# Performance work log

Measured on AMD Instinct MI355X. Metric: run time of the kernel, lower is better.

Reference implementation:

```python
import jax, jax.numpy as jnp
import numpy as np

N_NUC = 100_000
N_NN = 1_600_000
EMB = 128
MSG = 32
OUT = 128
LN_EPS = 1e-6  # flax LayerNorm default


def setup_inputs() -> dict:
    key = jax.random.key(0)
    ks = jax.random.split(key, 12)
    inp = {
        "s_embed": jax.random.normal(ks[0], (N_NUC, EMB), jnp.float32),
        "r_embed": jax.random.normal(ks[1], (N_NUC, EMB), jnp.float32),
        "e_embed": jax.random.normal(ks[2], (N_NN, MSG), jnp.float32),
        "norm": jax.random.uniform(ks[3], (N_NUC,), jnp.float32),
        "senders": jax.random.randint(ks[4], (N_NN,), 0, N_NUC, jnp.int32),
        "receivers": jax.random.randint(ks[5], (N_NN,), 0, N_NUC, jnp.int32),
        # learned parameters
        "W_s": jax.random.normal(ks[6], (EMB, MSG), jnp.float32) / np.sqrt(EMB),
        "b_s": jnp.zeros((MSG,), jnp.float32),
        "W_r": jax.random.normal(ks[7], (EMB, MSG), jnp.float32) / np.sqrt(EMB),
        "b_r": jnp.zeros((MSG,), jnp.float32),
        "ln_scale": jnp.ones((MSG,), jnp.float32),
        "ln_bias": jnp.zeros((MSG,), jnp.float32),
        "W_e": jax.random.normal(ks[8], (MSG, MSG), jnp.float32) / np.sqrt(MSG),
        "W_out": jax.random.normal(ks[9], (MSG, OUT), jnp.float32) / np.sqrt(MSG),
    }
    return inp


def _layernorm(x, scale, bias):
    mu = jnp.mean(x, axis=-1, keepdims=True)
    var = jnp.mean(jnp.square(x - mu), axis=-1, keepdims=True)
    return (x - mu) * jax.lax.rsqrt(var + LN_EPS) * scale + bias


def reference(s_embed, r_embed, e_embed, norm, senders, receivers,
              W_s, b_s, W_r, b_r, ln_scale, ln_bias, W_e, W_out):
    # Dense projections on nodes, then gather per edge: [n_nn, msg]
    inp = (s_embed @ W_s + b_s)[senders] + (r_embed @ W_r + b_r)[receivers]
    inp = _layernorm(inp, ln_scale, ln_bias)
    inp = jax.nn.silu(inp)
    inp = inp * (e_embed @ W_e)  # elementwise edge gating
    # scatter-add to receivers: [n_nuc, msg]
    msg = jax.ops.segment_sum(inp, receivers, num_segments=s_embed.shape[0])
    msg = msg * norm[:, None]
    return jax.nn.silu(msg @ W_out)
```

## Files before the change

### kernel.cpp

```cpp
#include <hip/hip_runtime.h>
#include <hip/hip_bf16.h>
#include <math.h>

#define N_NUC_C 100000
#define N_NN_C  1600000
#define EMB_C   128
#define MSG_C   32
#define OUT_C   128
#define NB1     98
#define NPART   8
#define R_PER_P (N_NUC_C / NPART)
#define SBLK    784
#define STHREADS (SBLK * 256)
#define LDS_USTR 17

__device__ __forceinline__ float silu_f(float y) {
    return y / (1.0f + __expf(-y));
}

__device__ __forceinline__ unsigned pack_bf16x2(float a, float b) {
    unsigned ua = __float_as_uint(a); ua += 0x7FFFu + ((ua >> 16) & 1u);
    unsigned ub = __float_as_uint(b); ub += 0x7FFFu + ((ub >> 16) & 1u);
    return (ua >> 16) | (ub & 0xFFFF0000u);
}

__global__ __launch_bounds__(256) void proj_kernel(
    const float* __restrict__ s_embed, const float* __restrict__ r_embed,
    const float* __restrict__ W_s, const float* __restrict__ b_s,
    const float* __restrict__ W_r, const float* __restrict__ b_r,
    float* __restrict__ proj )
{
    const int n   = blockIdx.x * blockDim.x + threadIdx.x;
    const int sub = blockIdx.y;
    const int pr  = sub >> 1;
    const int c0  = (sub & 1) * 16;
    if (n >= N_NUC_C) return;

    const float* __restrict__ src = pr ? r_embed : s_embed;
    const float* __restrict__ W   = pr ? W_r : W_s;
    const float* __restrict__ b   = pr ? b_r : b_s;
    float* __restrict__ dst = proj + (size_t)pr * N_NUC_C * MSG_C;

    float acc[16];
    #pragma unroll
    for (int i = 0; i < 16; ++i) acc[i] = b[c0 + i];

    const float* row = src + (size_t)n * EMB_C;
    #pragma unroll 4
    for (int k = 0; k < EMB_C; k += 4) {
        const float4 rv = *reinterpret_cast<const float4*>(row + k);
        #pragma unroll
        for (int i = 0; i < 16; ++i) {
            acc[i] = fmaf(rv.x, W[(k + 0) * MSG_C + c0 + i], acc[i]);
            acc[i] = fmaf(rv.y, W[(k + 1) * MSG_C + c0 + i], acc[i]);
            acc[i] = fmaf(rv.z, W[(k + 2) * MSG_C + c0 + i], acc[i]);
            acc[i] = fmaf(rv.w, W[(k + 3) * MSG_C + c0 + i], acc[i]);
        }
    }

    float4* d = reinterpret_cast<float4*>(dst + (size_t)n * MSG_C + c0);
    d[0] = make_float4(acc[0],  acc[1],  acc[2],  acc[3]);
    d[1] = make_float4(acc[4],  acc[5],  acc[6],  acc[7]);
    d[2] = make_float4(acc[8],  acc[9],  acc[10], acc[11]);
    d[3] = make_float4(acc[12], acc[13], acc[14], acc[15]);
}

__global__ __launch_bounds__(256) void rank_kernel(
    const int* __restrict__ receivers, int* __restrict__ cnt,
    int* __restrict__ rank)
{
    const int e = blockIdx.x * blockDim.x + threadIdx.x;
    if (e >= N_NN_C) return;
    rank[e] = atomicAdd(&cnt[receivers[e]], 1);
}

__global__ __launch_bounds__(256) void scan1_kernel(
    const int* __restrict__ cnt, int* __restrict__ excl, int* __restrict__ blockTot)
{
    __shared__ int waveTot[4];
    const int t = threadIdx.x, b = blockIdx.x;
    const int lane = t & 63, wid = t >> 6;
    const int base = b * 1024 + t * 4;

    int d0 = (base + 0 < N_NUC_C) ? cnt[base + 0] : 0;
    int d1 = (base + 1 < N_NUC_C) ? cnt[base + 1] : 0;
    int d2 = (base + 2 < N_NUC_C) ? cnt[base + 2] : 0;
    int d3 = (base + 3 < N_NUC_C) ? cnt[base + 3] : 0;
    const int s = d0 + d1 + d2 + d3;

    int incl = s;
    #pragma unroll
    for (int off = 1; off < 64; off <<= 1) {
        int v = __shfl_up(incl, off);
        if (lane >= off) incl += v;
    }
    const int wexcl = incl - s;
    if (lane == 63) waveTot[wid] = incl;
    __syncthreads();
    int wbase = 0;
    for (int w = 0; w < wid; ++w) wbase += waveTot[w];
    const int e0 = wbase + wexcl;

    if (base + 0 < N_NUC_C) excl[base + 0] = e0;
    if (base + 1 < N_NUC_C) excl[base + 1] = e0 + d0;
    if (base + 2 < N_NUC_C) excl[base + 2] = e0 + d0 + d1;
    if (base + 3 < N_NUC_C) excl[base + 3] = e0 + d0 + d1 + d2;
    if (t == 255) blockTot[b] = wbase + incl;
}

__global__ __launch_bounds__(128) void scan2_kernel(
    const int* __restrict__ blockTot, int* __restrict__ blockOff)
{
    __shared__ int sh[128];
    const int t = threadIdx.x;
    const int v = (t < NB1) ? blockTot[t] : 0;
    sh[t] = v;
    __syncthreads();
    #pragma unroll
    for (int off = 1; off < 128; off <<= 1) {
        int x = 0;
        if (t >= off) x = sh[t - off];
        __syncthreads();
        sh[t] += x;
        __syncthreads();
    }
    if (t < NB1) blockOff[t] = sh[t] - v;
}

__global__ __launch_bounds__(256) void scan3_kernel(
    const int* __restrict__ excl, const int* __restrict__ blockOff,
    int* __restrict__ offsets)
{
    const int n = blockIdx.x * blockDim.x + threadIdx.x;
    if (n < N_NUC_C) offsets[n] = excl[n] + blockOff[n >> 10];
    if (n == 0) offsets[N_NUC_C] = N_NN_C;
}

__global__ __launch_bounds__(256) void scatter_pack8_kernel(
    const int* __restrict__ senders, const int* __restrict__ receivers,
    const int* __restrict__ rank, const int* __restrict__ offsets,
    int4* __restrict__ edge_pack)
{
    const int p    = blockIdx.x & 7;
    const int blk  = blockIdx.x >> 3;
    const int base = blk * 256 + threadIdx.x;
    const int rlo  = p * R_PER_P;
    const int rhi  = rlo + R_PER_P;

    #pragma unroll
    for (int k = 0; k < 8; ++k) {
        const int e = base + k * STHREADS;
        if (e < N_NN_C) {
            const int r = receivers[e];
            if (r >= rlo && r < rhi) {
                const int dst = offsets[r] + rank[e];
                edge_pack[dst] = make_int4(e, senders[e], r, 0);
            }
        }
    }
}

__global__ __launch_bounds__(256) void fused_csr_kernel(
    const float* __restrict__ proj,
    const float* __restrict__ e_embed,
    const int4*  __restrict__ edge_pack,
    const int*   __restrict__ offsets,
    const float* __restrict__ ln_scale,
    const float* __restrict__ ln_bias,
    const float* __restrict__ W_e,
    float*       __restrict__ msg)
{
    __shared__ unsigned lds_u[256 * LDS_USTR];
    __shared__ int      lds_r[256];

    const int t  = threadIdx.x;
    const int B0 = blockIdx.x * 256;

    const int4 pk = edge_pack[B0 + t];
    const int e = pk.x, s = pk.y, r = pk.z;
    lds_r[t] = r;

    const float4* ee = reinterpret_cast<const float4*>(e_embed + (size_t)e * MSG_C);
    const float4* ps = reinterpret_cast<const float4*>(proj + (size_t)s * MSG_C);
    const float4* pq = reinterpret_cast<const float4*>(proj + (size_t)(N_NUC_C + r) * MSG_C);

    float ev[MSG_C], x[MSG_C];
    #pragma unroll
    for (int q = 0; q < 8; ++q) {
        const float4 v = ee[q];
        ev[4*q+0] = v.x; ev[4*q+1] = v.y; ev[4*q+2] = v.z; ev[4*q+3] = v.w;
    }
    #pragma unroll
    for (int q = 0; q < 8; ++q) {
        const float4 a = ps[q];
        const float4 b = pq[q];
        x[4*q+0] = a.x + b.x; x[4*q+1] = a.y + b.y;
        x[4*q+2] = a.z + b.z; x[4*q+3] = a.w + b.w;
    }

    float g[MSG_C];
    #pragma unroll
    for (int c = 0; c < MSG_C; ++c) g[c] = 0.0f;
    #pragma unroll
    for (int k = 0; k < MSG_C; ++k) {
        const float ek = ev[k];
        #pragma unroll
        for (int c = 0; c < MSG_C; ++c)
            g[c] = fmaf(ek, W_e[k * MSG_C + c], g[c]);
    }

    float mu = 0.0f;
    #pragma unroll
    for (int c = 0; c < MSG_C; ++c) mu += x[c];
    mu *= (1.0f / MSG_C);
    float var = 0.0f;
    #pragma unroll
    for (int c = 0; c < MSG_C; ++c) { const float d = x[c] - mu; var = fmaf(d, d, var); }
    var *= (1.0f / MSG_C);
    const float rs = rsqrtf(var + 1e-6f);

    unsigned* orow = &lds_u[t * LDS_USTR];
    #pragma unroll
    for (int i = 0; i < 16; ++i) {
        const int c0_ = 2*i, c1_ = 2*i + 1;
        const float y0 = (x[c0_] - mu) * rs * ln_scale[c0_] + ln_bias[c0_];
        const float y1 = (x[c1_] - mu) * rs * ln_scale[c1_] + ln_bias[c1_];
        orow[i] = pack_bf16x2(silu_f(y0) * g[c0_], silu_f(y1) * g[c1_]);
    }

    __syncthreads();

    const int r0 = lds_r[0];
    const int r1 = lds_r[255];
    const int total = (r1 - r0 + 1) << 5;

    for (int p = t; p < total; p += 256) {
        const int n  = r0 + (p >> 5);
        const int ch = p & 31;
        int b  = offsets[n];
        int en = offsets[n + 1];
        const bool interior = (b >= B0) && (en <= B0 + 256);
        if (b < B0) b = B0;
        if (en > B0 + 256) en = B0 + 256;

        const int dw  = ch >> 1;
        const bool hi = (ch & 1);
        float sum = 0.0f;
        for (int q = b - B0; q < en - B0; ++q) {
            const unsigned u = lds_u[q * LDS_USTR + dw];
            sum += __uint_as_float(hi ? (u & 0xFFFF0000u) : (u << 16));
        }

        float* dst = msg + (size_t)n * MSG_C + ch;
        if (interior)       *dst = sum;
        else if (en > b)    atomicAdd(dst, sum);
    }
}

__global__ __launch_bounds__(256) void edge_kernel(
    const float* __restrict__ proj, const float* __restrict__ e_embed,
    const int* __restrict__ senders, const int* __restrict__ receivers,
    const float* __restrict__ ln_scale, const float* __restrict__ ln_bias,
    const float* __restrict__ W_e, float* __restrict__ msg)
{
    const int e = blockIdx.x * blockDim.x + threadIdx.x;
    if (e >= N_NN_C) return;
    const int s = senders[e];
    const int r = receivers[e];
    const float4* ps = reinterpret_cast<const float4*>(proj + (size_t)s * MSG_C);
    const float4* pq = reinterpret_cast<const float4*>(proj + (size_t)(N_NUC_C + r) * MSG_C);
    float x[MSG_C];
    #pragma unroll
    for (int q = 0; q < 8; ++q) {
        const float4 a = ps[q];
        const float4 b = pq[q];
        x[4*q+0] = a.x + b.x; x[4*q+1] = a.y + b.y;
        x[4*q+2] = a.z + b.z; x[4*q+3] = a.w + b.w;
    }
    float mu = 0.0f;
    #pragma unroll
    for (int c = 0; c < MSG_C; ++c) mu += x[c];
    mu *= (1.0f / MSG_C);
    float var = 0.0f;
    #pragma unroll
    for (int c = 0; c < MSG_C; ++c) { const float d = x[c] - mu; var = fmaf(d, d, var); }
    var *= (1.0f / MSG_C);
    const float rs = rsqrtf(var + 1e-6f);
    #pragma unroll
    for (int c = 0; c < MSG_C; ++c) {
        const float y = (x[c] - mu) * rs * ln_scale[c] + ln_bias[c];
        x[c] = silu_f(y);
    }
    float ev[MSG_C];
    const float4* ee = reinterpret_cast<const float4*>(e_embed + (size_t)e * MSG_C);
    #pragma unroll
    for (int q = 0; q < 8; ++q) {
        const float4 v = ee[q];
        ev[4*q+0] = v.x; ev[4*q+1] = v.y; ev[4*q+2] = v.z; ev[4*q+3] = v.w;
    }
    float g[MSG_C];
    #pragma unroll
    for (int c = 0; c < MSG_C; ++c) g[c] = 0.0f;
    #pragma unroll
    for (int k = 0; k < MSG_C; ++k) {
        const float ek = ev[k];
        #pragma unroll
        for (int c = 0; c < MSG_C; ++c) g[c] = fmaf(ek, W_e[k * MSG_C + c], g[c]);
    }
    float* mrow = msg + (size_t)r * MSG_C;
    #pragma unroll
    for (int c = 0; c < MSG_C; ++c) atomicAdd(mrow + c, x[c] * g[c]);
}

__global__ __launch_bounds__(256) void out_kernel(
    const float* __restrict__ msg, const float* __restrict__ norm,
    const float* __restrict__ W_out, float* __restrict__ out)
{
    const int j     = threadIdx.x & (OUT_C - 1);
    const int local = threadIdx.x >> 7;

    float w[MSG_C];
    #pragma unroll
    for (int k = 0; k < MSG_C; ++k) w[k] = W_out[k * OUT_C + j];

    for (int n = blockIdx.x * 2 + local; n < N_NUC_C; n += gridDim.x * 2) {
        const float4* m4 = reinterpret_cast<const float4*>(msg + (size_t)n * MSG_C);
        float acc = 0.0f;
        #pragma unroll
        for (int q = 0; q < 8; ++q) {
            const float4 mv = m4[q];
            acc = fmaf(mv.x, w[4*q+0], acc);
            acc = fmaf(mv.y, w[4*q+1], acc);
            acc = fmaf(mv.z, w[4*q+2], acc);
            acc = fmaf(mv.w, w[4*q+3], acc);
        }
        acc *= norm[n];
        out[(size_t)n * OUT_C + j] = silu_f(acc);
    }
}

extern "C" void kernel_launch(void* const* d_in, const int* in_sizes, int n_in,
                              void* d_out, int out_size, void* d_ws, size_t ws_size,
                              hipStream_t stream) {
    const float* s_embed   = (const float*)d_in[0];
    const float* r_embed   = (const float*)d_in[1];
    const float* e_embed   = (const float*)d_in[2];
    const float* norm      = (const float*)d_in[3];
    const int*   senders   = (const int*)d_in[4];
    const int*   receivers = (const int*)d_in[5];
    const float* W_s       = (const float*)d_in[6];
    const float* b_s       = (const float*)d_in[7];
    const float* W_r       = (const float*)d_in[8];
    const float* b_r       = (const float*)d_in[9];
    const float* ln_scale  = (const float*)d_in[10];
    const float* ln_bias   = (const float*)d_in[11];
    const float* W_e       = (const float*)d_in[12];
    const float* W_out     = (const float*)d_in[13];
    float* out = (float*)d_out;

    char* ws = (char*)d_ws;
    size_t off = 0;
    auto alloc = [&](size_t bytes) { char* p = ws + off; off += (bytes + 255) & ~(size_t)255; return p; };

    float* proj      = (float*)alloc((size_t)2 * N_NUC_C * MSG_C * 4);
    float* msg       = (float*)alloc((size_t)N_NUC_C * MSG_C * 4);
    const size_t off_min = off;
    int*   cnt       = (int*)  alloc((size_t)N_NUC_C * 4);
    int*   excl      = (int*)  alloc((size_t)N_NUC_C * 4);
    int*   offsets   = (int*)  alloc((size_t)(N_NUC_C + 1) * 4);
    int*   blockTot  = (int*)  alloc(128 * 4);
    int*   blockOff  = (int*)  alloc(128 * 4);
    int*   rank      = (int*)  alloc((size_t)N_NN_C * 4);
    int4*  edge_pack = (int4*) alloc((size_t)N_NN_C * 16);
    const size_t off_full = off;

    dim3 pgrid((N_NUC_C + 255) / 256, 4);
    proj_kernel<<<pgrid, 256, 0, stream>>>(s_embed, r_embed, W_s, b_s, W_r, b_r, proj);

    if (off_full <= ws_size) {
        hipMemsetAsync(cnt, 0, (size_t)N_NUC_C * 4, stream);
        hipMemsetAsync(msg, 0, (size_t)N_NUC_C * MSG_C * 4, stream);
        rank_kernel<<<(N_NN_C + 255) / 256, 256, 0, stream>>>(receivers, cnt, rank);
        scan1_kernel<<<NB1, 256, 0, stream>>>(cnt, excl, blockTot);
        scan2_kernel<<<1, 128, 0, stream>>>(blockTot, blockOff);
        scan3_kernel<<<(N_NUC_C + 255) / 256, 256, 0, stream>>>(excl, blockOff, offsets);
        scatter_pack8_kernel<<<NPART * SBLK, 256, 0, stream>>>(
            senders, receivers, rank, offsets, edge_pack);
        fused_csr_kernel<<<N_NN_C / 256, 256, 0, stream>>>(
            proj, e_embed, edge_pack, offsets, ln_scale, ln_bias, W_e, msg);
    } else if (off_min <= ws_size) {
        hipMemsetAsync(msg, 0, (size_t)N_NUC_C * MSG_C * 4, stream);
        edge_kernel<<<(N_NN_C + 255) / 256, 256, 0, stream>>>(
            proj, e_embed, senders, receivers, ln_scale, ln_bias, W_e, msg);
    }

    out_kernel<<<2048, 256, 0, stream>>>(msg, norm, W_out, out);
}
```

Baseline: 364.8 us.

## Replace per-edge rank array with partitioned counting and atomic cursor scatter

The count pass is now partitioned by receiver range, like the scatter pass, so each block's atomics hit one eighth of the count array and stay cache-local. It no longer writes a per-edge rank array. The scatter pass takes its slot from an atomic increment on a per-node cursor seeded from the offsets, which removes the rank read and the offsets gather. The cost is a second atomic per edge in the scatter, and the order of edges within a node becomes nondeterministic, which can change the summation order in the fused CSR kernel.

```diff
diff --git a/kernel.cpp b/kernel.cpp
--- a/kernel.cpp
+++ b/kernel.cpp
@@ -65,13 +65,24 @@
     d[3] = make_float4(acc[12], acc[13], acc[14], acc[15]);
 }
 
-__global__ __launch_bounds__(256) void rank_kernel(
-    const int* __restrict__ receivers, int* __restrict__ cnt,
-    int* __restrict__ rank)
-{
-    const int e = blockIdx.x * blockDim.x + threadIdx.x;
-    if (e >= N_NN_C) return;
-    rank[e] = atomicAdd(&cnt[receivers[e]], 1);
+__global__ __launch_bounds__(256) void count8_kernel(
+    const int* __restrict__ receivers, int* __restrict__ cnt)
+{
+    const int p    = blockIdx.x & 7;
+    const int blk  = blockIdx.x >> 3;
+    const int base = blk * 256 + threadIdx.x;
+    const int rlo  = p * R_PER_P;
+    const int rhi  = rlo + R_PER_P;
+
+    #pragma unroll
+    for (int k = 0; k < 8; ++k) {
+        const int e = base + k * STHREADS;
+        if (e < N_NN_C) {
+            const int r = receivers[e];
+            if (r >= rlo && r < rhi)
+                atomicAdd(&cnt[r], 1);
+        }
+    }
 }
 
 __global__ __launch_bounds__(256) void scan1_kernel(
@@ -129,17 +140,20 @@
 
 __global__ __launch_bounds__(256) void scan3_kernel(
     const int* __restrict__ excl, const int* __restrict__ blockOff,
-    int* __restrict__ offsets)
+    int* __restrict__ offsets, int* __restrict__ cursor)
 {
     const int n = blockIdx.x * blockDim.x + threadIdx.x;
-    if (n < N_NUC_C) offsets[n] = excl[n] + blockOff[n >> 10];
+    if (n < N_NUC_C) {
+        const int v = excl[n] + blockOff[n >> 10];
+        offsets[n] = v;
+        cursor[n]  = v;
+    }
     if (n == 0) offsets[N_NUC_C] = N_NN_C;
 }
 
 __global__ __launch_bounds__(256) void scatter_pack8_kernel(
     const int* __restrict__ senders, const int* __restrict__ receivers,
-    const int* __restrict__ rank, const int* __restrict__ offsets,
-    int4* __restrict__ edge_pack)
+    int* __restrict__ cursor, int4* __restrict__ edge_pack)
 {
     const int p    = blockIdx.x & 7;
     const int blk  = blockIdx.x >> 3;
@@ -153,7 +167,7 @@
         if (e < N_NN_C) {
             const int r = receivers[e];
             if (r >= rlo && r < rhi) {
-                const int dst = offsets[r] + rank[e];
+                const int dst = atomicAdd(&cursor[r], 1);
                 edge_pack[dst] = make_int4(e, senders[e], r, 0);
             }
         }
@@ -368,9 +382,9 @@
     int*   cnt       = (int*)  alloc((size_t)N_NUC_C * 4);
     int*   excl      = (int*)  alloc((size_t)N_NUC_C * 4);
     int*   offsets   = (int*)  alloc((size_t)(N_NUC_C + 1) * 4);
+    int*   cursor    = (int*)  alloc((size_t)N_NUC_C * 4);
     int*   blockTot  = (int*)  alloc(128 * 4);
     int*   blockOff  = (int*)  alloc(128 * 4);
-    int*   rank      = (int*)  alloc((size_t)N_NN_C * 4);
     int4*  edge_pack = (int4*) alloc((size_t)N_NN_C * 16);
     const size_t off_full = off;
 
@@ -380,12 +394,12 @@
     if (off_full <= ws_size) {
         hipMemsetAsync(cnt, 0, (size_t)N_NUC_C * 4, stream);
         hipMemsetAsync(msg, 0, (size_t)N_NUC_C * MSG_C * 4, stream);
-        rank_kernel<<<(N_NN_C + 255) / 256, 256, 0, stream>>>(receivers, cnt, rank);
+        count8_kernel<<<NPART * SBLK, 256, 0, stream>>>(receivers, cnt);
         scan1_kernel<<<NB1, 256, 0, stream>>>(cnt, excl, blockTot);
         scan2_kernel<<<1, 128, 0, stream>>>(blockTot, blockOff);
-        scan3_kernel<<<(N_NUC_C + 255) / 256, 256, 0, stream>>>(excl, blockOff, offsets);
+        scan3_kernel<<<(N_NUC_C + 255) / 256, 256, 0, stream>>>(excl, blockOff, offsets, cursor);
         scatter_pack8_kernel<<<NPART * SBLK, 256, 0, stream>>>(
-            senders, receivers, rank, offsets, edge_pack);
+            senders, receivers, cursor, edge_pack);
         fused_csr_kernel<<<N_NN_C / 256, 256, 0, stream>>>(
             proj, e_embed, edge_pack, offsets, ln_scale, ln_bias, W_e, msg);
     } else if (off_min <= ws_size) {
```

Measured after the change: 389.5 us. 6.8% more time.

## Compute edge gating matvec with bf16 MFMA via LDS staging

Applied to the files above, without the earlier changes.

The per-thread scalar 32x32 FMA loop that computes e_embed @ W_e is replaced. Each thread now packs its edge-embedding row to bf16 in shared memory, and each wavefront runs 16x16x32 bf16 MFMA tiles against W_e fragments held in registers. The gate values are written back to shared memory as bf16 and unpacked per thread. This removes about 1k scalar FMAs per edge and the register array that held the edge row. In exchange it adds two block barriers and extra LDS traffic, and it rounds e_embed, W_e and the gate values to bf16.

```diff
diff --git a/kernel.cpp b/kernel.cpp
--- a/kernel.cpp
+++ b/kernel.cpp
@@ -14,6 +14,9 @@
 #define STHREADS (SBLK * 256)
 #define LDS_USTR 17
 
+typedef __attribute__((ext_vector_type(8))) short bf16x8;
+typedef __attribute__((ext_vector_type(4))) float f32x4;
+
 __device__ __forceinline__ float silu_f(float y) {
     return y / (1.0f + __expf(-y));
 }
@@ -22,6 +25,11 @@
     unsigned ua = __float_as_uint(a); ua += 0x7FFFu + ((ua >> 16) & 1u);
     unsigned ub = __float_as_uint(b); ub += 0x7FFFu + ((ub >> 16) & 1u);
     return (ua >> 16) | (ub & 0xFFFF0000u);
+}
+
+__device__ __forceinline__ unsigned short bf16_of(float a) {
+    unsigned ua = __float_as_uint(a); ua += 0x7FFFu + ((ua >> 16) & 1u);
+    return (unsigned short)(ua >> 16);
 }
 
 __global__ __launch_bounds__(256) void proj_kernel(
@@ -170,26 +178,83 @@
     const float* __restrict__ W_e,
     float*       __restrict__ msg)
 {
-    __shared__ unsigned lds_u[256 * LDS_USTR];
+    __shared__ unsigned lds_ev[256 * LDS_USTR];
+    __shared__ unsigned lds_g [256 * LDS_USTR];
     __shared__ int      lds_r[256];
 
-    const int t  = threadIdx.x;
-    const int B0 = blockIdx.x * 256;
+    const int t    = threadIdx.x;
+    const int lane = t & 63;
+    const int wb   = t & ~63;
+    const int B0   = blockIdx.x * 256;
 
     const int4 pk = edge_pack[B0 + t];
     const int e = pk.x, s = pk.y, r = pk.z;
     lds_r[t] = r;
 
-    const float4* ee = reinterpret_cast<const float4*>(e_embed + (size_t)e * MSG_C);
+    {
+        const float4* ee = reinterpret_cast<const float4*>(e_embed + (size_t)e * MSG_C);
+        unsigned* evrow = &lds_ev[t * LDS_USTR];
+        #pragma unroll
+        for (int q = 0; q < 8; ++q) {
+            const float4 v = ee[q];
+            evrow[2*q+0] = pack_bf16x2(v.x, v.y);
+            evrow[2*q+1] = pack_bf16x2(v.z, v.w);
+        }
+    }
+
+    bf16x8 bf0, bf1;
+    {
+        const int kg = (lane >> 4) * 8;
+        const int n0 = lane & 15;
+        #pragma unroll
+        for (int i = 0; i < 8; ++i) {
+            bf0[i] = (short)bf16_of(W_e[(kg + i) * MSG_C + n0]);
+            bf1[i] = (short)bf16_of(W_e[(kg + i) * MSG_C + 16 + n0]);
+        }
+    }
+
+    __syncthreads();
+
+    {
+        unsigned short* g16 = reinterpret_cast<unsigned short*>(lds_g);
+        #pragma unroll
+        for (int mt = 0; mt < 4; ++mt) {
+            const int arow = wb + mt * 16 + (lane & 15);
+            const unsigned* ar = &lds_ev[arow * LDS_USTR + ((lane >> 4) << 2)];
+            const unsigned u0 = ar[0], u1 = ar[1], u2 = ar[2], u3 = ar[3];
+            bf16x8 af;
+            af[0] = (short)(u0 & 0xFFFFu); af[1] = (short)(u0 >> 16);
+            af[2] = (short)(u1 & 0xFFFFu); af[3] = (short)(u1 >> 16);
+            af[4] = (short)(u2 & 0xFFFFu); af[5] = (short)(u2 >> 16);
+            af[6] = (short)(u3 & 0xFFFFu); af[7] = (short)(u3 >> 16);
+            f32x4 z = {0.f, 0.f, 0.f, 0.f};
+            const f32x4 a0 = __builtin_amdgcn_mfma_f32_16x16x32_bf16(af, bf0, z, 0, 0, 0);
+            const f32x4 a1 = __builtin_amdgcn_mfma_f32_16x16x32_bf16(af, bf1, z, 0, 0, 0);
+            const int rbase = wb + mt * 16 + ((lane >> 4) << 2);
+            #pragma unroll
+            for (int rg = 0; rg < 4; ++rg) {
+                g16[(rbase + rg) * (2 * LDS_USTR) + (lane & 15)]      = bf16_of(a0[rg]);
+                g16[(rbase + rg) * (2 * LDS_USTR) + 16 + (lane & 15)] = bf16_of(a1[rg]);
+            }
+        }
+    }
+
+    __syncthreads();
+
+    float g[MSG_C];
+    {
+        const unsigned* gr = &lds_g[t * LDS_USTR];
+        #pragma unroll
+        for (int j = 0; j < 16; ++j) {
+            const unsigned u = gr[j];
+            g[2*j]   = __uint_as_float(u << 16);
+            g[2*j+1] = __uint_as_float(u & 0xFFFF0000u);
+        }
+    }
+
     const float4* ps = reinterpret_cast<const float4*>(proj + (size_t)s * MSG_C);
     const float4* pq = reinterpret_cast<const float4*>(proj + (size_t)(N_NUC_C + r) * MSG_C);
-
-    float ev[MSG_C], x[MSG_C];
-    #pragma unroll
-    for (int q = 0; q < 8; ++q) {
-        const float4 v = ee[q];
-        ev[4*q+0] = v.x; ev[4*q+1] = v.y; ev[4*q+2] = v.z; ev[4*q+3] = v.w;
-    }
+    float x[MSG_C];
     #pragma unroll
     for (int q = 0; q < 8; ++q) {
         const float4 a = ps[q];
@@ -198,17 +263,6 @@
         x[4*q+2] = a.z + b.z; x[4*q+3] = a.w + b.w;
     }
 
-    float g[MSG_C];
-    #pragma unroll
-    for (int c = 0; c < MSG_C; ++c) g[c] = 0.0f;
-    #pragma unroll
-    for (int k = 0; k < MSG_C; ++k) {
-        const float ek = ev[k];
-        #pragma unroll
-        for (int c = 0; c < MSG_C; ++c)
-            g[c] = fmaf(ek, W_e[k * MSG_C + c], g[c]);
-    }
-
     float mu = 0.0f;
     #pragma unroll
     for (int c = 0; c < MSG_C; ++c) mu += x[c];
@@ -219,7 +273,7 @@
     var *= (1.0f / MSG_C);
     const float rs = rsqrtf(var + 1e-6f);
 
-    unsigned* orow = &lds_u[t * LDS_USTR];
+    unsigned* orow = &lds_ev[t * LDS_USTR];
     #pragma unroll
     for (int i = 0; i < 16; ++i) {
         const int c0_ = 2*i, c1_ = 2*i + 1;
@@ -247,7 +301,7 @@
         const bool hi = (ch & 1);
         float sum = 0.0f;
         for (int q = b - B0; q < en - B0; ++q) {
-            const unsigned u = lds_u[q * LDS_USTR + dw];
+            const unsigned u = lds_ev[q * LDS_USTR + dw];
             sum += __uint_as_float(hi ? (u & 0xFFFF0000u) : (u << 16));
         }
 
```

After: 347.7 us. 1.05x faster.
